# Kernel optimization log

Hardware: AMD Instinct MI355X
Metric: run time of the kernel (lower is better)

## Reference

```python
import jax, jax.numpy as jnp
import numpy as np

N_NODES = 50000
N_EDGES = 800000
FEAT = 256
HID = 64
OUT = 40


def setup_inputs() -> dict:
    key = jax.random.key(0)
    ks = jax.random.split(key, 5)
    x = jax.random.normal(ks[0], (N_NODES, FEAT), dtype=jnp.float32)
    edge_index = jax.random.randint(ks[1], (2, N_EDGES), 0, N_NODES, dtype=jnp.int64)
    # Glorot-style init for GCN linear weights
    W1 = jax.random.normal(ks[2], (FEAT, HID), dtype=jnp.float32) * (1.0 / np.sqrt(FEAT))
    b1 = jnp.zeros((HID,), dtype=jnp.float32)
    W2 = jax.random.normal(ks[3], (HID, OUT), dtype=jnp.float32) * (1.0 / np.sqrt(HID))
    b2 = jnp.zeros((OUT,), dtype=jnp.float32)
    return {"x": x, "edge_index": edge_index, "W1": W1, "b1": b1, "W2": W2, "b2": b2}


def _gcn_conv(h, W, b, src, dst, norm, n_nodes):
    # GCNConv: linear transform first (reduces message width), then
    # symmetric-normalized gather-scale-scatter aggregation.
    h = h @ W  # [N, out]
    msg = h[src] * norm[:, None]  # [E+N, out] gather + scale
    agg = jax.ops.segment_sum(msg, dst, num_segments=n_nodes)  # scatter-add
    return agg + b


def reference(x, edge_index, W1, b1, W2, b2):
    n = x.shape[0]
    # add self loops (GCNConv default add_self_loops=True)
    loops = jnp.arange(n, dtype=edge_index.dtype)
    src = jnp.concatenate([edge_index[0], loops])
    dst = jnp.concatenate([edge_index[1], loops])
    # symmetric normalization: deg computed on A + I (in-degree at dst)
    deg = jax.ops.segment_sum(jnp.ones_like(dst, dtype=x.dtype), dst, num_segments=n)
    dinv = jax.lax.rsqrt(deg)  # deg >= 1 due to self loops
    norm = dinv[src] * dinv[dst]  # [E+N]

    h = jax.nn.relu(_gcn_conv(x, W1, b1, src, dst, norm, n))
    # dropout is identity in eval mode (reference baseline)
    h = _gcn_conv(h, W2, b2, src, dst, norm, n)
    return jax.nn.log_softmax(h, axis=1)
```

## Files before the change

### kernel.cpp

```cpp
#include <hip/hip_runtime.h>
#include <hip/hip_bf16.h>


constexpr int NN   = 50000;
constexpr int NNP  = 50048;
constexpr int ZR   = 50000;
constexpr int NE   = 800000;
constexpr int FEAT = 256;
constexpr int HID  = 64;
constexpr int OUTD = 40;
constexpr int NC   = (NN + 255) / 256;
constexpr int FCH  = 2048;
constexpr int NCH  = (NE + FCH - 1) / FCH;

typedef short bf16x8 __attribute__((ext_vector_type(8)));
typedef float f32x4  __attribute__((ext_vector_type(4)));

__device__ __forceinline__ float b2f(__hip_bfloat16 v) { return __bfloat162float(v); }
__device__ __forceinline__ float bflo(unsigned u) { return __uint_as_float(u << 16); }
__device__ __forceinline__ float bfhi(unsigned u) { return __uint_as_float(u & 0xffff0000u); }
__device__ __forceinline__ unsigned short f2bu(float f) {
    __hip_bfloat16 h = __float2bfloat16(f);
    return *(unsigned short*)&h;
}
__device__ __forceinline__ unsigned pack2bf(float a, float b) {
    return (unsigned)f2bu(a) | ((unsigned)f2bu(b) << 16);
}
__device__ __forceinline__ float loadF(const void* p, int i, bool f32) {
    return f32 ? ((const float*)p)[i] : b2f(((const __hip_bfloat16*)p)[i]);
}
__device__ __forceinline__ int loadE(const int* ei, int e, int row, bool i64) {
    long long idx = (long long)row * NE + e;
    return i64 ? ei[2 * idx] : ei[idx];
}
__device__ __forceinline__ bf16x8 pack8(float4 a, float4 b) {
    bf16x8 r;
    r[0] = (short)f2bu(a.x); r[1] = (short)f2bu(a.y);
    r[2] = (short)f2bu(a.z); r[3] = (short)f2bu(a.w);
    r[4] = (short)f2bu(b.x); r[5] = (short)f2bu(b.y);
    r[6] = (short)f2bu(b.z); r[7] = (short)f2bu(b.w);
    return r;
}

__global__ __launch_bounds__(256) void k_zero(const unsigned* __restrict__ xw,
                                              const int* __restrict__ ew,
                                              int* flags, int* cnt,
                                              unsigned* __restrict__ h2pad) {
    int i = blockIdx.x * 256 + threadIdx.x;
    if (i < NN) cnt[i] = 0;
    if (blockIdx.x == 0 && threadIdx.x < 20) h2pad[threadIdx.x] = 0;
    if (blockIdx.x == 0 && threadIdx.x == 0) {
        int outliers = 0;
        for (int k = 0; k < 256; k++) {
            int e = (xw[k] >> 7) & 0xFF;
            if (e < 100 || e > 140) outliers++;
        }
        flags[0] = (outliers > 64) ? 1 : 0;
        int nz = 0;
        for (int k = 1; k < 64; k += 2)
            if (ew[k] != 0) nz++;
        flags[1] = (nz == 0) ? 1 : 0;
    }
}

__global__ __launch_bounds__(256) void k_hist(const int* __restrict__ ei,
                                              const int* __restrict__ flags,
                                              int* cnt, int* __restrict__ rank) {
    const bool i64 = flags[1] != 0;
    int e = blockIdx.x * 256 + threadIdx.x;
    if (e < NE) rank[e] = atomicAdd(&cnt[loadE(ei, e, 1, i64)], 1);
}
__global__ __launch_bounds__(256) void k_scan1(const int* __restrict__ cnt,
                                               int* row_start, int* partial, float* dinv) {
    __shared__ int s[256];
    int t = threadIdx.x, i = blockIdx.x * 256 + t;
    int v = (i < NN) ? cnt[i] : 0;
    if (i < NN) dinv[i] = rsqrtf(1.0f + (float)v);
    s[t] = v;
    __syncthreads();
    for (int off = 1; off < 256; off <<= 1) {
        int tmp = (t >= off) ? s[t - off] : 0;
        __syncthreads();
        s[t] += tmp;
        __syncthreads();
    }
    if (i < NN) row_start[i] = s[t] - v;
    if (t == 255) partial[blockIdx.x] = s[255];
}
__global__ __launch_bounds__(256) void k_scan2p(const int* __restrict__ partial, int* pp) {
    __shared__ int s[256];
    int t = threadIdx.x;
    int v = (t < NC) ? partial[t] : 0;
    s[t] = v;
    __syncthreads();
    for (int off = 1; off < 256; off <<= 1) {
        int tmp = (t >= off) ? s[t - off] : 0;
        __syncthreads();
        s[t] += tmp;
        __syncthreads();
    }
    pp[t] = s[t] - v;
}
__global__ __launch_bounds__(256) void k_fill(const int* __restrict__ ei,
                                              const int* __restrict__ flags,
                                              const int* __restrict__ row_start,
                                              const int* __restrict__ pp,
                                              const int* __restrict__ rank,
                                              unsigned short* __restrict__ csr16) {
    const bool i64 = flags[1] != 0;
    const int cls = blockIdx.x & 7;
    const int e0 = (blockIdx.x >> 3) * FCH;
#pragma unroll
    for (int k = 0; k < FCH / 256; k++) {
        int e = e0 + k * 256 + threadIdx.x;
        if (e < NE) {
            int d = loadE(ei, e, 1, i64);
            if (d / 6250 == cls) {
                int s = loadE(ei, e, 0, i64);
                csr16[row_start[d] + pp[d >> 8] + rank[e]] = (unsigned short)s;
            }
        }
    }
}

__global__ __launch_bounds__(256) void k_gemm1(const void* __restrict__ xb,
                                               const void* __restrict__ W1,
                                               const float* __restrict__ dinv,
                                               const int* __restrict__ flags,
                                               unsigned short* __restrict__ h1u) {
    __shared__ __align__(16) unsigned short wt16[64 * 264];
    const bool f32 = flags[0] != 0;
    const int t = threadIdx.x;
    if (f32) {
        const float* wf = (const float*)W1;
        for (int i = t * 4; i < FEAT * HID; i += 1024) {
            float4 w = *(const float4*)(wf + i);
            int k = i >> 6, n0 = i & 63;
            wt16[(n0 + 0) * 264 + k] = f2bu(w.x);
            wt16[(n0 + 1) * 264 + k] = f2bu(w.y);
            wt16[(n0 + 2) * 264 + k] = f2bu(w.z);
            wt16[(n0 + 3) * 264 + k] = f2bu(w.w);
        }
    } else {
        const unsigned short* wu = (const unsigned short*)W1;
        for (int i = t * 4; i < FEAT * HID; i += 1024) {
            ushort4 w = *(const ushort4*)(wu + i);
            int k = i >> 6, n0 = i & 63;
            wt16[(n0 + 0) * 264 + k] = w.x;
            wt16[(n0 + 1) * 264 + k] = w.y;
            wt16[(n0 + 2) * 264 + k] = w.z;
            wt16[(n0 + 3) * 264 + k] = w.w;
        }
    }
    const int wv = t >> 6, lane = t & 63, l15 = lane & 15, quad = lane >> 4;
    const int gr = blockIdx.x * 64 + wv * 16 + l15;
    const bool rowok = gr < NN;
    f32x4 acc[4];
#pragma unroll
    for (int nt = 0; nt < 4; nt++) acc[nt] = (f32x4){0.f, 0.f, 0.f, 0.f};
    __syncthreads();

    if (f32) {
        const float* xr = (const float*)xb + (size_t)gr * FEAT + quad * 8;
        float4 z4 = make_float4(0, 0, 0, 0);
        float4 c0 = rowok ? *(const float4*)xr : z4;
        float4 c1 = rowok ? *(const float4*)(xr + 4) : z4;
#pragma unroll
        for (int ks = 0; ks < 8; ks++) {
            float4 n0 = z4, n1 = z4;
            if (ks < 7 && rowok) {
                n0 = *(const float4*)(xr + (ks + 1) * 32);
                n1 = *(const float4*)(xr + (ks + 1) * 32 + 4);
            }
            bf16x8 a = pack8(c0, c1);
            const unsigned short* wk = wt16 + ks * 32 + quad * 8;
#pragma unroll
            for (int nt = 0; nt < 4; nt++) {
                bf16x8 b = *(const bf16x8*)(wk + (size_t)(nt * 16 + l15) * 264);
                acc[nt] = __builtin_amdgcn_mfma_f32_16x16x32_bf16(a, b, acc[nt], 0, 0, 0);
            }
            c0 = n0; c1 = n1;
        }
    } else {
        const unsigned short* xr = (const unsigned short*)xb + (size_t)gr * FEAT + quad * 8;
        bf16x8 zz = (bf16x8){0, 0, 0, 0, 0, 0, 0, 0};
        bf16x8 cur = rowok ? *(const bf16x8*)xr : zz;
#pragma unroll
        for (int ks = 0; ks < 8; ks++) {
            bf16x8 nxt = zz;
            if (ks < 7 && rowok) nxt = *(const bf16x8*)(xr + (ks + 1) * 32);
            const unsigned short* wk = wt16 + ks * 32 + quad * 8;
#pragma unroll
            for (int nt = 0; nt < 4; nt++) {
                bf16x8 b = *(const bf16x8*)(wk + (size_t)(nt * 16 + l15) * 264);
                acc[nt] = __builtin_amdgcn_mfma_f32_16x16x32_bf16(cur, b, acc[nt], 0, 0, 0);
            }
            cur = nxt;
        }
    }
    const int rbase = blockIdx.x * 64 + wv * 16 + quad * 4;
    float dv[4];
#pragma unroll
    for (int r = 0; r < 4; r++) dv[r] = (rbase + r < NN) ? dinv[rbase + r] : 0.f;
#pragma unroll
    for (int r = 0; r < 4; r++) {
        int grow = rbase + r;
#pragma unroll
        for (int nt = 0; nt < 4; nt++)
            h1u[(size_t)grow * HID + nt * 16 + l15] = f2bu(acc[nt][r] * dv[r]);
    }
}

__global__ __launch_bounds__(256, 4) void k_gather1f(const uint2* __restrict__ h1v,
                                                  const float* __restrict__ dinv,
                                                  const int* __restrict__ row_start,
                                                  const int* __restrict__ pp,
                                                  const int* __restrict__ cnt,
                                                  const unsigned short* __restrict__ csr16,
                                                  const void* __restrict__ W2,
                                                  const void* __restrict__ b1,
                                                  const int* __restrict__ flags,
                                                  unsigned short* __restrict__ h2u) {
    __shared__ __align__(16) float w2t[OUTD * 68];
    __shared__ __align__(16) float gbuf[16 * 68];
    __shared__ float dns[16];
    const bool f32 = flags[0] != 0;
    const int t = threadIdx.x;
    for (int i = t; i < HID * OUTD; i += 256) {
        int c = i >> 6, k = i & 63;
        w2t[c * 68 + k] = loadF(W2, (size_t)k * OUTD + c, f32);
    }
    const int nl = t >> 4, l16 = t & 15;
    const int n = blockIdx.x * 16 + nl;
    const float dn = dinv[n];
    uint2 u0 = h1v[n * 16 + l16];
    float a0 = bflo(u0.x), a1 = bfhi(u0.x), a2 = bflo(u0.y), a3 = bfhi(u0.y);
    float e0 = 0.f, e1 = 0.f, e2 = 0.f, e3 = 0.f;
    const int rs = row_start[n] + pp[n >> 8], c = cnt[n];
    for (int base = 0; base < c; base += 16) {
        int rem = c - base;
        int sv = (l16 < rem) ? (int)csr16[rs + base + l16] : ZR;
        uint2 b[8], d[8];
#pragma unroll
        for (int j = 0; j < 8; j++) {
            int s = __shfl(sv, j, 16);
            b[j] = h1v[(s << 4) | l16];
        }
#pragma unroll
        for (int j = 0; j < 8; j++) {
            int s = __shfl(sv, j + 8, 16);
            d[j] = h1v[(s << 4) | l16];
        }
#pragma unroll
        for (int j = 0; j < 8; j++) {
            a0 += bflo(b[j].x); a1 += bfhi(b[j].x);
            a2 += bflo(b[j].y); a3 += bfhi(b[j].y);
            e0 += bflo(d[j].x); e1 += bfhi(d[j].x);
            e2 += bflo(d[j].y); e3 += bfhi(d[j].y);
        }
    }
    int cb = 4 * l16;
    float g0 = fmaxf(dn * (a0 + e0) + loadF(b1, cb, f32), 0.f);
    float g1 = fmaxf(dn * (a1 + e1) + loadF(b1, cb + 1, f32), 0.f);
    float g2 = fmaxf(dn * (a2 + e2) + loadF(b1, cb + 2, f32), 0.f);
    float g3 = fmaxf(dn * (a3 + e3) + loadF(b1, cb + 3, f32), 0.f);
    *(float4*)(gbuf + nl * 68 + cb) = make_float4(g0, g1, g2, g3);
    if (l16 == 0) dns[nl] = dn;
    __syncthreads();
    for (int idx = t; idx < 16 * OUTD; idx += 256) {
        int node = idx / OUTD, col = idx % OUTD;
        const float4* gp = (const float4*)(gbuf + node * 68);
        const float4* wp = (const float4*)(w2t + col * 68);
        float o = 0.f;
#pragma unroll 4
        for (int k4 = 0; k4 < 16; k4++) {
            float4 a = gp[k4], b = wp[k4];
            o += a.x * b.x + a.y * b.y + a.z * b.z + a.w * b.w;
        }
        h2u[(size_t)(blockIdx.x * 16 + node) * OUTD + col] = f2bu(o * dns[node]);
    }
}

__global__ __launch_bounds__(256, 4) void k_gather2(const uint2* __restrict__ h2v,
                                                 const float* __restrict__ dinv,
                                                 const int* __restrict__ row_start,
                                                 const int* __restrict__ pp,
                                                 const int* __restrict__ cnt,
                                                 const unsigned short* __restrict__ csr16,
                                                 const void* __restrict__ b2,
                                                 const int* __restrict__ flags,
                                                 void* __restrict__ out) {
    const bool f32 = flags[0] != 0;
    const int t = threadIdx.x;
    const int nl = t >> 4, l16 = t & 15;
    const int n = blockIdx.x * 16 + nl;
    const bool act = l16 < 10;
    const float dn = dinv[n];
    const int lclamp = act ? l16 : 9;
    uint2 u0 = h2v[n * 10 + lclamp];
    float a0 = bflo(u0.x), a1 = bfhi(u0.x), a2 = bflo(u0.y), a3 = bfhi(u0.y);
    float e0 = 0.f, e1 = 0.f, e2 = 0.f, e3 = 0.f;
    const int rs = row_start[n] + pp[n >> 8], c = cnt[n];
    for (int base = 0; base < c; base += 16) {
        int rem = c - base;
        int sv = (l16 < rem) ? (int)csr16[rs + base + l16] : ZR;
        uint2 b[8], d[8];
#pragma unroll
        for (int j = 0; j < 8; j++) {
            int s = __shfl(sv, j, 16);
            b[j] = h2v[s * 10 + lclamp];
        }
#pragma unroll
        for (int j = 0; j < 8; j++) {
            int s = __shfl(sv, j + 8, 16);
            d[j] = h2v[s * 10 + lclamp];
        }
#pragma unroll
        for (int j = 0; j < 8; j++) {
            a0 += bflo(b[j].x); a1 += bfhi(b[j].x);
            a2 += bflo(b[j].y); a3 += bfhi(b[j].y);
            e0 += bflo(d[j].x); e1 += bfhi(d[j].x);
            e2 += bflo(d[j].y); e3 += bfhi(d[j].y);
        }
    }
    int cb = 4 * l16;
    float v0 = -3.0e38f, v1 = -3.0e38f, v2 = -3.0e38f, v3 = -3.0e38f;
    if (act) {
        v0 = dn * (a0 + e0) + loadF(b2, cb, f32);
        v1 = dn * (a1 + e1) + loadF(b2, cb + 1, f32);
        v2 = dn * (a2 + e2) + loadF(b2, cb + 2, f32);
        v3 = dn * (a3 + e3) + loadF(b2, cb + 3, f32);
    }
    float mx = fmaxf(fmaxf(v0, v1), fmaxf(v2, v3));
#pragma unroll
    for (int off = 8; off; off >>= 1) mx = fmaxf(mx, __shfl_xor(mx, off, 16));
    float ev = act ? expf(v0 - mx) + expf(v1 - mx) + expf(v2 - mx) + expf(v3 - mx) : 0.f;
#pragma unroll
    for (int off = 8; off; off >>= 1) ev += __shfl_xor(ev, off, 16);
    float lg = logf(ev);
    if (act) {
        float r0 = v0 - mx - lg, r1 = v1 - mx - lg;
        float r2 = v2 - mx - lg, r3 = v3 - mx - lg;
        if (f32) {
            *(float4*)((float*)out + (size_t)n * OUTD + cb) = make_float4(r0, r1, r2, r3);
        } else {
            ((uint2*)out)[(size_t)n * 10 + l16] = make_uint2(pack2bf(r0, r1), pack2bf(r2, r3));
        }
    }
}

extern "C" void kernel_launch(void* const* d_in, const int* in_sizes, int n_in,
                              void* d_out, int out_size, void* d_ws, size_t ws_size,
                              hipStream_t stream) {
    const void* x  = d_in[0];
    const int*  ei = (const int*)d_in[1];
    const void* W1 = d_in[2];
    const void* b1 = d_in[3];
    const void* W2 = d_in[4];
    const void* b2 = d_in[5];

    float* ws        = (float*)d_ws;
    int*   flags     = (int*)ws;
    float* dinv      = ws + 16;
    int*   cnt       = (int*)(dinv + 50048);
    int*   row_start = cnt + 50048;
    int*   partial   = row_start + 50048;
    int*   pp        = partial + 256;
    int*   rank      = pp + 256;
    unsigned short* csr16 = (unsigned short*)(rank + NE);
    unsigned short* h1u   = csr16 + NE;
    unsigned short* h2u   = h1u + (size_t)NNP * HID;
    unsigned* h2pad = (unsigned*)(h2u + (size_t)ZR * OUTD);

    k_zero  <<<(NN + 255) / 256, 256, 0, stream>>>((const unsigned*)x, ei, flags, cnt, h2pad);
    k_hist  <<<(NE + 255) / 256, 256, 0, stream>>>(ei, flags, cnt, rank);
    k_scan1 <<<NC, 256, 0, stream>>>(cnt, row_start, partial, dinv);
    k_scan2p<<<1, 256, 0, stream>>>(partial, pp);
    k_fill  <<<NCH * 8, 256, 0, stream>>>(ei, flags, row_start, pp, rank, csr16);
    k_gemm1 <<<NNP / 64, 256, 0, stream>>>(x, W1, dinv, flags, h1u);
    k_gather1f<<<NN / 16, 256, 0, stream>>>((const uint2*)h1u, dinv, row_start, pp, cnt, csr16,
                                            W2, b1, flags, h2u);
    k_gather2<<<NN / 16, 256, 0, stream>>>((const uint2*)h2u, dinv, row_start, pp, cnt, csr16,
                                           b2, flags, d_out);
}
```

Before: 229.8 us.

## Split layer-1 gather into two feature-half passes and hoist gather2 loads

The layer-1 aggregation is split into two kernels, each gathering one 32-feature half of h1. The first pass stores its relu output as fp16 in a scratch buffer that reuses the rank array; the second gathers the other half, merges both and applies W2. The intent is a smaller working set per pass so the gathered rows stay resident in cache. The cost is a second traversal of the CSR plus an extra launch and intermediate write. Separately, gather2 issues all 16 neighbour loads before any accumulation, with a sched_barrier to keep them grouped and raise memory-level parallelism.

New measurement: 240.7 us. 4.7% more time.

```diff
diff --git a/kernel.cpp b/kernel.cpp
--- a/kernel.cpp
+++ b/kernel.cpp
@@ -1,5 +1,6 @@
 #include <hip/hip_runtime.h>
 #include <hip/hip_bf16.h>
+#include <hip/hip_fp16.h>
 
 
 constexpr int NN   = 50000;
@@ -25,6 +26,20 @@
 }
 __device__ __forceinline__ unsigned pack2bf(float a, float b) {
     return (unsigned)f2bu(a) | ((unsigned)f2bu(b) << 16);
+}
+__device__ __forceinline__ unsigned pack2h(float a, float b) {
+    __half ha = __float2half(a), hb = __float2half(b);
+    return (unsigned)*(unsigned short*)&ha | ((unsigned)*(unsigned short*)&hb << 16);
+}
+__device__ __forceinline__ float h2flo(unsigned u) {
+    unsigned short s = (unsigned short)(u & 0xffff);
+    __half h = *(__half*)&s;
+    return __half2float(h);
+}
+__device__ __forceinline__ float h2fhi(unsigned u) {
+    unsigned short s = (unsigned short)(u >> 16);
+    __half h = *(__half*)&s;
+    return __half2float(h);
 }
 __device__ __forceinline__ float loadF(const void* p, int i, bool f32) {
     return f32 ? ((const float*)p)[i] : b2f(((const __hip_bfloat16*)p)[i]);
@@ -211,16 +226,62 @@
     }
 }
 
-__global__ __launch_bounds__(256, 4) void k_gather1f(const uint2* __restrict__ h1v,
-                                                  const float* __restrict__ dinv,
-                                                  const int* __restrict__ row_start,
-                                                  const int* __restrict__ pp,
-                                                  const int* __restrict__ cnt,
-                                                  const unsigned short* __restrict__ csr16,
-                                                  const void* __restrict__ W2,
-                                                  const void* __restrict__ b1,
-                                                  const int* __restrict__ flags,
-                                                  unsigned short* __restrict__ h2u) {
+__global__ __launch_bounds__(256, 4) void k_g1p0(const unsigned* __restrict__ h1d,
+                                                 const float* __restrict__ dinv,
+                                                 const int* __restrict__ row_start,
+                                                 const int* __restrict__ pp,
+                                                 const int* __restrict__ cnt,
+                                                 const unsigned short* __restrict__ csr16,
+                                                 const void* __restrict__ b1,
+                                                 const int* __restrict__ flags,
+                                                 unsigned* __restrict__ g32) {
+    const bool f32 = flags[0] != 0;
+    const int t = threadIdx.x;
+    const int nl = t >> 4, l16 = t & 15;
+    const int n = blockIdx.x * 16 + nl;
+    const float dn = dinv[n];
+    const int po = l16;
+    unsigned u0 = h1d[n * 32 + po];
+    float a0 = bflo(u0), a1 = bfhi(u0);
+    float e0 = 0.f, e1 = 0.f;
+    const int rs = row_start[n] + pp[n >> 8], c = cnt[n];
+    for (int base = 0; base < c; base += 16) {
+        int rem = c - base;
+        int sv = (l16 < rem) ? (int)csr16[rs + base + l16] : ZR;
+        unsigned b[8], d[8];
+#pragma unroll
+        for (int j = 0; j < 8; j++) {
+            int s = __shfl(sv, j, 16);
+            b[j] = h1d[(s << 5) + po];
+        }
+#pragma unroll
+        for (int j = 0; j < 8; j++) {
+            int s = __shfl(sv, j + 8, 16);
+            d[j] = h1d[(s << 5) + po];
+        }
+#pragma unroll
+        for (int j = 0; j < 8; j++) {
+            a0 += bflo(b[j]); a1 += bfhi(b[j]);
+            e0 += bflo(d[j]); e1 += bfhi(d[j]);
+        }
+    }
+    int cb = 2 * l16;
+    float g0 = fmaxf(dn * (a0 + e0) + loadF(b1, cb, f32), 0.f);
+    float g1 = fmaxf(dn * (a1 + e1) + loadF(b1, cb + 1, f32), 0.f);
+    g32[n * 16 + l16] = pack2h(g0, g1);
+}
+
+__global__ __launch_bounds__(256, 4) void k_g1p1(const unsigned* __restrict__ h1d,
+                                                 const float* __restrict__ dinv,
+                                                 const int* __restrict__ row_start,
+                                                 const int* __restrict__ pp,
+                                                 const int* __restrict__ cnt,
+                                                 const unsigned short* __restrict__ csr16,
+                                                 const void* __restrict__ W2,
+                                                 const void* __restrict__ b1,
+                                                 const int* __restrict__ flags,
+                                                 const unsigned* __restrict__ g32,
+                                                 unsigned short* __restrict__ h2u) {
     __shared__ __align__(16) float w2t[OUTD * 68];
     __shared__ __align__(16) float gbuf[16 * 68];
     __shared__ float dns[16];
@@ -233,38 +294,39 @@
     const int nl = t >> 4, l16 = t & 15;
     const int n = blockIdx.x * 16 + nl;
     const float dn = dinv[n];
-    uint2 u0 = h1v[n * 16 + l16];
-    float a0 = bflo(u0.x), a1 = bfhi(u0.x), a2 = bflo(u0.y), a3 = bfhi(u0.y);
-    float e0 = 0.f, e1 = 0.f, e2 = 0.f, e3 = 0.f;
+    const int po = 16 + l16;
+    unsigned u0 = h1d[n * 32 + po];
+    float a0 = bflo(u0), a1 = bfhi(u0);
+    float e0 = 0.f, e1 = 0.f;
     const int rs = row_start[n] + pp[n >> 8], c = cnt[n];
     for (int base = 0; base < c; base += 16) {
         int rem = c - base;
         int sv = (l16 < rem) ? (int)csr16[rs + base + l16] : ZR;
-        uint2 b[8], d[8];
+        unsigned b[8], d[8];
 #pragma unroll
         for (int j = 0; j < 8; j++) {
             int s = __shfl(sv, j, 16);
-            b[j] = h1v[(s << 4) | l16];
+            b[j] = h1d[(s << 5) + po];
         }
 #pragma unroll
         for (int j = 0; j < 8; j++) {
             int s = __shfl(sv, j + 8, 16);
-            d[j] = h1v[(s << 4) | l16];
-        }
-#pragma unroll
-        for (int j = 0; j < 8; j++) {
-            a0 += bflo(b[j].x); a1 += bfhi(b[j].x);
-            a2 += bflo(b[j].y); a3 += bfhi(b[j].y);
-            e0 += bflo(d[j].x); e1 += bfhi(d[j].x);
-            e2 += bflo(d[j].y); e3 += bfhi(d[j].y);
-        }
-    }
-    int cb = 4 * l16;
-    float g0 = fmaxf(dn * (a0 + e0) + loadF(b1, cb, f32), 0.f);
-    float g1 = fmaxf(dn * (a1 + e1) + loadF(b1, cb + 1, f32), 0.f);
-    float g2 = fmaxf(dn * (a2 + e2) + loadF(b1, cb + 2, f32), 0.f);
-    float g3 = fmaxf(dn * (a3 + e3) + loadF(b1, cb + 3, f32), 0.f);
-    *(float4*)(gbuf + nl * 68 + cb) = make_float4(g0, g1, g2, g3);
+            d[j] = h1d[(s << 5) + po];
+        }
+#pragma unroll
+        for (int j = 0; j < 8; j++) {
+            a0 += bflo(b[j]); a1 += bfhi(b[j]);
+            e0 += bflo(d[j]); e1 += bfhi(d[j]);
+        }
+    }
+    int cb = 32 + 2 * l16;
+    float g2 = fmaxf(dn * (a0 + e0) + loadF(b1, cb, f32), 0.f);
+    float g3 = fmaxf(dn * (a1 + e1) + loadF(b1, cb + 1, f32), 0.f);
+    unsigned pk = g32[n * 16 + l16];
+    gbuf[nl * 68 + 2 * l16]     = h2flo(pk);
+    gbuf[nl * 68 + 2 * l16 + 1] = h2fhi(pk);
+    gbuf[nl * 68 + cb]     = g2;
+    gbuf[nl * 68 + cb + 1] = g3;
     if (l16 == 0) dns[nl] = dn;
     __syncthreads();
     for (int idx = t; idx < 16 * OUTD; idx += 256) {
@@ -304,24 +366,39 @@
     for (int base = 0; base < c; base += 16) {
         int rem = c - base;
         int sv = (l16 < rem) ? (int)csr16[rs + base + l16] : ZR;
-        uint2 b[8], d[8];
-#pragma unroll
-        for (int j = 0; j < 8; j++) {
-            int s = __shfl(sv, j, 16);
-            b[j] = h2v[s * 10 + lclamp];
-        }
-#pragma unroll
-        for (int j = 0; j < 8; j++) {
-            int s = __shfl(sv, j + 8, 16);
-            d[j] = h2v[s * 10 + lclamp];
-        }
-#pragma unroll
-        for (int j = 0; j < 8; j++) {
-            a0 += bflo(b[j].x); a1 += bfhi(b[j].x);
-            a2 += bflo(b[j].y); a3 += bfhi(b[j].y);
-            e0 += bflo(d[j].x); e1 += bfhi(d[j].x);
-            e2 += bflo(d[j].y); e3 += bfhi(d[j].y);
-        }
+        int s0  = __shfl(sv, 0, 16),  s1  = __shfl(sv, 1, 16);
+        int s2  = __shfl(sv, 2, 16),  s3  = __shfl(sv, 3, 16);
+        int s4  = __shfl(sv, 4, 16),  s5  = __shfl(sv, 5, 16);
+        int s6  = __shfl(sv, 6, 16),  s7  = __shfl(sv, 7, 16);
+        int s8  = __shfl(sv, 8, 16),  s9  = __shfl(sv, 9, 16);
+        int s10 = __shfl(sv, 10, 16), s11 = __shfl(sv, 11, 16);
+        int s12 = __shfl(sv, 12, 16), s13 = __shfl(sv, 13, 16);
+        int s14 = __shfl(sv, 14, 16), s15 = __shfl(sv, 15, 16);
+        uint2 b0  = h2v[s0  * 10 + lclamp], b1_ = h2v[s1  * 10 + lclamp];
+        uint2 b2_ = h2v[s2  * 10 + lclamp], b3_ = h2v[s3  * 10 + lclamp];
+        uint2 b4_ = h2v[s4  * 10 + lclamp], b5_ = h2v[s5  * 10 + lclamp];
+        uint2 b6_ = h2v[s6  * 10 + lclamp], b7_ = h2v[s7  * 10 + lclamp];
+        uint2 d0  = h2v[s8  * 10 + lclamp], d1  = h2v[s9  * 10 + lclamp];
+        uint2 d2  = h2v[s10 * 10 + lclamp], d3  = h2v[s11 * 10 + lclamp];
+        uint2 d4  = h2v[s12 * 10 + lclamp], d5  = h2v[s13 * 10 + lclamp];
+        uint2 d6  = h2v[s14 * 10 + lclamp], d7  = h2v[s15 * 10 + lclamp];
+        __builtin_amdgcn_sched_barrier(0);
+        a0 += bflo(b0.x);  a1 += bfhi(b0.x);  a2 += bflo(b0.y);  a3 += bfhi(b0.y);
+        a0 += bflo(b1_.x); a1 += bfhi(b1_.x); a2 += bflo(b1_.y); a3 += bfhi(b1_.y);
+        a0 += bflo(b2_.x); a1 += bfhi(b2_.x); a2 += bflo(b2_.y); a3 += bfhi(b2_.y);
+        a0 += bflo(b3_.x); a1 += bfhi(b3_.x); a2 += bflo(b3_.y); a3 += bfhi(b3_.y);
+        a0 += bflo(b4_.x); a1 += bfhi(b4_.x); a2 += bflo(b4_.y); a3 += bfhi(b4_.y);
+        a0 += bflo(b5_.x); a1 += bfhi(b5_.x); a2 += bflo(b5_.y); a3 += bfhi(b5_.y);
+        a0 += bflo(b6_.x); a1 += bfhi(b6_.x); a2 += bflo(b6_.y); a3 += bfhi(b6_.y);
+        a0 += bflo(b7_.x); a1 += bfhi(b7_.x); a2 += bflo(b7_.y); a3 += bfhi(b7_.y);
+        e0 += bflo(d0.x);  e1 += bfhi(d0.x);  e2 += bflo(d0.y);  e3 += bfhi(d0.y);
+        e0 += bflo(d1.x);  e1 += bfhi(d1.x);  e2 += bflo(d1.y);  e3 += bfhi(d1.y);
+        e0 += bflo(d2.x);  e1 += bfhi(d2.x);  e2 += bflo(d2.y);  e3 += bfhi(d2.y);
+        e0 += bflo(d3.x);  e1 += bfhi(d3.x);  e2 += bflo(d3.y);  e3 += bfhi(d3.y);
+        e0 += bflo(d4.x);  e1 += bfhi(d4.x);  e2 += bflo(d4.y);  e3 += bfhi(d4.y);
+        e0 += bflo(d5.x);  e1 += bfhi(d5.x);  e2 += bflo(d5.y);  e3 += bfhi(d5.y);
+        e0 += bflo(d6.x);  e1 += bfhi(d6.x);  e2 += bflo(d6.y);  e3 += bfhi(d6.y);
+        e0 += bflo(d7.x);  e1 += bfhi(d7.x);  e2 += bflo(d7.y);  e3 += bfhi(d7.y);
     }
     int cb = 4 * l16;
     float v0 = -3.0e38f, v1 = -3.0e38f, v2 = -3.0e38f, v3 = -3.0e38f;
@@ -371,6 +448,7 @@
     unsigned short* h1u   = csr16 + NE;
     unsigned short* h2u   = h1u + (size_t)NNP * HID;
     unsigned* h2pad = (unsigned*)(h2u + (size_t)ZR * OUTD);
+    unsigned* g32   = (unsigned*)rank;
 
     k_zero  <<<(NN + 255) / 256, 256, 0, stream>>>((const unsigned*)x, ei, flags, cnt, h2pad);
     k_hist  <<<(NE + 255) / 256, 256, 0, stream>>>(ei, flags, cnt, rank);
@@ -378,8 +456,10 @@
     k_scan2p<<<1, 256, 0, stream>>>(partial, pp);
     k_fill  <<<NCH * 8, 256, 0, stream>>>(ei, flags, row_start, pp, rank, csr16);
     k_gemm1 <<<NNP / 64, 256, 0, stream>>>(x, W1, dinv, flags, h1u);
-    k_gather1f<<<NN / 16, 256, 0, stream>>>((const uint2*)h1u, dinv, row_start, pp, cnt, csr16,
-                                            W2, b1, flags, h2u);
+    k_g1p0  <<<NN / 16, 256, 0, stream>>>((const unsigned*)h1u, dinv, row_start, pp, cnt,
+                                          csr16, b1, flags, g32);
+    k_g1p1  <<<NN / 16, 256, 0, stream>>>((const unsigned*)h1u, dinv, row_start, pp, cnt,
+                                          csr16, W2, b1, flags, g32, h2u);
     k_gather2<<<NN / 16, 256, 0, stream>>>((const uint2*)h2u, dinv, row_start, pp, cnt, csr16,
                                            b2, flags, d_out);
 }
```

## Store layer-2 features as fp8 with 64B rows and add cache-warm pass

Applied to the files above, without the earlier changes.

Layer-2 transformed features are now written as fp8 (4 per 32-bit word) in 64-byte-padded rows instead of bf16 80-byte rows. The second gather then reads one dword per lane and unpacks with hardware fp8 conversion, cutting gather traffic and aligning rows to cache lines. A new k_warm kernel streams the whole fp8 buffer once beforehand to pull it into cache. fp8 cuts the precision of the aggregated logits and may break tolerance. The warm-up adds a launch and a pass over the buffer that does no useful arithmetic.

New measurement: 233.9 us. No clear change (+1.8%).

```diff
diff --git a/kernel.cpp b/kernel.cpp
--- a/kernel.cpp
+++ b/kernel.cpp
@@ -15,6 +15,7 @@
 
 typedef short bf16x8 __attribute__((ext_vector_type(8)));
 typedef float f32x4  __attribute__((ext_vector_type(4)));
+typedef float f32x2  __attribute__((ext_vector_type(2)));
 
 __device__ __forceinline__ float b2f(__hip_bfloat16 v) { return __bfloat162float(v); }
 __device__ __forceinline__ float bflo(unsigned u) { return __uint_as_float(u << 16); }
@@ -42,13 +43,49 @@
     return r;
 }
 
+#if __has_builtin(__builtin_amdgcn_cvt_pk_f32_fp8) && __has_builtin(__builtin_amdgcn_cvt_pk_fp8_f32)
+__device__ __forceinline__ void unpack_fp8x4(unsigned u, float& f0, float& f1,
+                                             float& f2, float& f3) {
+    f32x2 lo = __builtin_amdgcn_cvt_pk_f32_fp8((int)u, false);
+    f32x2 hi = __builtin_amdgcn_cvt_pk_f32_fp8((int)u, true);
+    f0 = lo[0]; f1 = lo[1]; f2 = hi[0]; f3 = hi[1];
+}
+__device__ __forceinline__ unsigned pack_fp8x4(float a, float b, float c, float d) {
+    int v = 0;
+    v = __builtin_amdgcn_cvt_pk_fp8_f32(a, b, v, false);
+    v = __builtin_amdgcn_cvt_pk_fp8_f32(c, d, v, true);
+    return (unsigned)v;
+}
+#else
+__device__ __forceinline__ float dec8(unsigned b) {
+    return __uint_as_float(((b & 0x80u) << 24) | ((b & 0x7fu) << 20)) * 0x1p120f;
+}
+__device__ __forceinline__ void unpack_fp8x4(unsigned u, float& f0, float& f1,
+                                             float& f2, float& f3) {
+    f0 = dec8(u & 0xff); f1 = dec8((u >> 8) & 0xff);
+    f2 = dec8((u >> 16) & 0xff); f3 = dec8(u >> 24);
+}
+__device__ __forceinline__ unsigned enc8(float f) {
+    float a = fabsf(f) * 0x1p-120f;
+    unsigned ub = __float_as_uint(a);
+    unsigned lsb = (ub >> 20) & 1u;
+    ub += 0x7FFFFu + lsb;
+    unsigned v = (ub >> 20) & 0x7fu;
+    if (v > 0x7e) v = 0x7e;
+    return v | ((__float_as_uint(f) >> 24) & 0x80u);
+}
+__device__ __forceinline__ unsigned pack_fp8x4(float a, float b, float c, float d) {
+    return enc8(a) | (enc8(b) << 8) | (enc8(c) << 16) | (enc8(d) << 24);
+}
+#endif
+
 __global__ __launch_bounds__(256) void k_zero(const unsigned* __restrict__ xw,
                                               const int* __restrict__ ew,
                                               int* flags, int* cnt,
                                               unsigned* __restrict__ h2pad) {
     int i = blockIdx.x * 256 + threadIdx.x;
     if (i < NN) cnt[i] = 0;
-    if (blockIdx.x == 0 && threadIdx.x < 20) h2pad[threadIdx.x] = 0;
+    if (blockIdx.x == 0 && threadIdx.x < 16) h2pad[threadIdx.x] = 0;
     if (blockIdx.x == 0 && threadIdx.x == 0) {
         int outliers = 0;
         for (int k = 0; k < 256; k++) {
@@ -220,9 +257,10 @@
                                                   const void* __restrict__ W2,
                                                   const void* __restrict__ b1,
                                                   const int* __restrict__ flags,
-                                                  unsigned short* __restrict__ h2u) {
+                                                  unsigned* __restrict__ h2f) {
     __shared__ __align__(16) float w2t[OUTD * 68];
     __shared__ __align__(16) float gbuf[16 * 68];
+    __shared__ __align__(16) float obuf[16][40];
     __shared__ float dns[16];
     const bool f32 = flags[0] != 0;
     const int t = threadIdx.x;
@@ -277,11 +315,31 @@
             float4 a = gp[k4], b = wp[k4];
             o += a.x * b.x + a.y * b.y + a.z * b.z + a.w * b.w;
         }
-        h2u[(size_t)(blockIdx.x * 16 + node) * OUTD + col] = f2bu(o * dns[node]);
-    }
-}
-
-__global__ __launch_bounds__(256, 4) void k_gather2(const uint2* __restrict__ h2v,
+        obuf[node][col] = o * dns[node];
+    }
+    __syncthreads();
+    if (t < 160) {
+        int node = t / 10, dw = t % 10;
+        const float* op = obuf[node] + dw * 4;
+        h2f[(blockIdx.x * 16 + node) * 16 + dw] =
+            pack_fp8x4(op[0], op[1], op[2], op[3]);
+    }
+}
+
+__global__ __launch_bounds__(256) void k_warm(const uint4* __restrict__ h2q, int* flags) {
+    const int total4 = NNP * 4;
+    const int per = (total4 + 63) / 64;
+    const int s = blockIdx.x >> 3;
+    const int lo = s * per, hi = min(lo + per, total4);
+    unsigned acc = 0;
+    for (int i = lo + threadIdx.x; i < hi; i += 256) {
+        uint4 v = h2q[i];
+        acc += v.x ^ v.y ^ v.z ^ v.w;
+    }
+    if (acc == 0x9e3779b9u) flags[15] = (int)acc;
+}
+
+__global__ __launch_bounds__(256, 4) void k_gather2(const unsigned* __restrict__ h2f,
                                                  const float* __restrict__ dinv,
                                                  const int* __restrict__ row_start,
                                                  const int* __restrict__ pp,
@@ -297,30 +355,31 @@
     const bool act = l16 < 10;
     const float dn = dinv[n];
     const int lclamp = act ? l16 : 9;
-    uint2 u0 = h2v[n * 10 + lclamp];
-    float a0 = bflo(u0.x), a1 = bfhi(u0.x), a2 = bflo(u0.y), a3 = bfhi(u0.y);
+    float a0, a1, a2, a3;
+    unpack_fp8x4(h2f[n * 16 + lclamp], a0, a1, a2, a3);
     float e0 = 0.f, e1 = 0.f, e2 = 0.f, e3 = 0.f;
     const int rs = row_start[n] + pp[n >> 8], c = cnt[n];
     for (int base = 0; base < c; base += 16) {
         int rem = c - base;
         int sv = (l16 < rem) ? (int)csr16[rs + base + l16] : ZR;
-        uint2 b[8], d[8];
+        unsigned b[8], d[8];
 #pragma unroll
         for (int j = 0; j < 8; j++) {
             int s = __shfl(sv, j, 16);
-            b[j] = h2v[s * 10 + lclamp];
+            b[j] = h2f[(s << 4) + lclamp];
         }
 #pragma unroll
         for (int j = 0; j < 8; j++) {
             int s = __shfl(sv, j + 8, 16);
-            d[j] = h2v[s * 10 + lclamp];
-        }
-#pragma unroll
-        for (int j = 0; j < 8; j++) {
-            a0 += bflo(b[j].x); a1 += bfhi(b[j].x);
-            a2 += bflo(b[j].y); a3 += bfhi(b[j].y);
-            e0 += bflo(d[j].x); e1 += bfhi(d[j].x);
-            e2 += bflo(d[j].y); e3 += bfhi(d[j].y);
+            d[j] = h2f[(s << 4) + lclamp];
+        }
+#pragma unroll
+        for (int j = 0; j < 8; j++) {
+            float x0, x1, x2, x3, y0, y1, y2, y3;
+            unpack_fp8x4(b[j], x0, x1, x2, x3);
+            unpack_fp8x4(d[j], y0, y1, y2, y3);
+            a0 += x0; a1 += x1; a2 += x2; a3 += x3;
+            e0 += y0; e1 += y1; e2 += y2; e3 += y3;
         }
     }
     int cb = 4 * l16;
@@ -369,8 +428,8 @@
     int*   rank      = pp + 256;
     unsigned short* csr16 = (unsigned short*)(rank + NE);
     unsigned short* h1u   = csr16 + NE;
-    unsigned short* h2u   = h1u + (size_t)NNP * HID;
-    unsigned* h2pad = (unsigned*)(h2u + (size_t)ZR * OUTD);
+    unsigned* h2f   = (unsigned*)(h1u + (size_t)NNP * HID);
+    unsigned* h2pad = h2f + (size_t)ZR * 16;
 
     k_zero  <<<(NN + 255) / 256, 256, 0, stream>>>((const unsigned*)x, ei, flags, cnt, h2pad);
     k_hist  <<<(NE + 255) / 256, 256, 0, stream>>>(ei, flags, cnt, rank);
@@ -379,7 +438,8 @@
     k_fill  <<<NCH * 8, 256, 0, stream>>>(ei, flags, row_start, pp, rank, csr16);
     k_gemm1 <<<NNP / 64, 256, 0, stream>>>(x, W1, dinv, flags, h1u);
     k_gather1f<<<NN / 16, 256, 0, stream>>>((const uint2*)h1u, dinv, row_start, pp, cnt, csr16,
-                                            W2, b1, flags, h2u);
-    k_gather2<<<NN / 16, 256, 0, stream>>>((const uint2*)h2u, dinv, row_start, pp, cnt, csr16,
+                                            W2, b1, flags, h2f);
+    k_warm  <<<512, 256, 0, stream>>>((const uint4*)h2f, flags);
+    k_gather2<<<NN / 16, 256, 0, stream>>>(h2f, dinv, row_start, pp, cnt, csr16,
                                            b2, flags, d_out);
 }
```
